# Kernel optimization log

Hardware: AMD Instinct MI355X
Metric: run time of the kernel (lower is better)

Reference implementation:

```python
import jax, jax.numpy as jnp
import numpy as np

B, N, C = 2, 32768, 512
L, H = 64, 8
DH = C // H
NB = N // L
EG_HID = 16


def setup_inputs() -> dict:
    key = jax.random.key(0)
    ks = jax.random.split(key, 12)
    x = jax.random.normal(ks[0], (B, N, C), dtype=jnp.float32)
    attn_mask = jax.random.randint(ks[1], (NB, L, L), 0, 2, dtype=jnp.int32)
    edge_feats = jax.random.normal(ks[2], (NB, L, L, 4), dtype=jnp.float32)
    s = 1.0 / np.sqrt(C)
    w_qkv = jax.random.normal(ks[3], (C, 3 * C), dtype=jnp.float32) * s
    b_qkv = jnp.zeros((3 * C,), dtype=jnp.float32)
    w_proj = jax.random.normal(ks[4], (C, C), dtype=jnp.float32) * s
    b_proj = jnp.zeros((C,), dtype=jnp.float32)
    w_eg1 = jax.random.normal(ks[5], (4, EG_HID), dtype=jnp.float32) * 0.01
    b_eg1 = jnp.zeros((EG_HID,), dtype=jnp.float32)
    w_eg2 = jax.random.normal(ks[6], (EG_HID, H), dtype=jnp.float32) * 0.01
    b_eg2 = jnp.zeros((H,), dtype=jnp.float32)
    w_blk = jax.random.normal(ks[7], (C, H), dtype=jnp.float32) * 0.01
    b_blk = jnp.zeros((H,), dtype=jnp.float32)
    return {"x": x, "attn_mask": attn_mask, "edge_feats": edge_feats,
            "w_qkv": w_qkv, "b_qkv": b_qkv, "w_proj": w_proj, "b_proj": b_proj,
            "w_eg1": w_eg1, "b_eg1": b_eg1, "w_eg2": w_eg2, "b_eg2": b_eg2,
            "w_blk": w_blk, "b_blk": b_blk}


def reference(x, attn_mask, edge_feats, w_qkv, b_qkv, w_proj, b_proj,
              w_eg1, b_eg1, w_eg2, b_eg2, w_blk, b_blk):
    scale = DH ** -0.5
    x_blk = x.reshape(B, NB, L, C)
    # bias_physics: (B, NB, L, L, 4), expanded across batch
    bias = jnp.broadcast_to(edge_feats[None], (B, NB, L, L, 4))
    idx = jnp.arange(L)
    # zero diagonal, set channel 3 of diagonal to 1
    bias = bias.at[:, :, idx, idx, :].set(0.0)
    bias = bias.at[:, :, idx, idx, 3].set(1.0)
    # mask: (B, NB, L, L); ensure each query row attends to at least itself
    mask = jnp.broadcast_to(attn_mask[None], (B, NB, L, L))
    need_diag = (mask.sum(axis=-1) < 1).astype(mask.dtype)  # (B, NB, L)
    diag = mask[:, :, idx, idx]
    mask = mask.at[:, :, idx, idx].set(jnp.maximum(diag, need_diag))
    # qkv
    qkv = x_blk @ w_qkv + b_qkv  # (B, NB, L, 3C)
    q = qkv[..., :C].reshape(B, NB, L, H, DH)
    k = qkv[..., C:2 * C].reshape(B, NB, L, H, DH)
    v = qkv[..., 2 * C:].reshape(B, NB, L, H, DH)
    scores = jnp.einsum('bnqhd,bnkhd->bnqkh', q, k) * scale
    scores = scores + bias[..., 3:4]
    mask_e = (mask[..., None] == 0)  # (B, NB, L, L, 1)
    scores = jnp.where(mask_e, -jnp.inf, scores)
    attn_probs = jax.nn.softmax(scores, axis=3)
    # edge-gate MLP: 4 -> 16 (exact GELU) -> H
    gate = jax.nn.gelu(bias @ w_eg1 + b_eg1, approximate=False) @ w_eg2 + b_eg2
    gate = jnp.where(mask_e, 0.0, gate)
    combined = attn_probs + gate
    x_mid = jnp.einsum('bnqkh,bnkhd->bnqhd', combined, v)  # (B, NB, L, H, DH)
    # block route token
    block_node = x_blk.mean(axis=2, keepdims=True)  # (B, NB, 1, C)
    v_block = (block_node @ w_qkv + b_qkv)[..., 2 * C:].reshape(B, NB, 1, H, DH)
    g_block = jax.nn.sigmoid(x_blk @ w_blk + b_blk)  # (B, NB, L, H)
    x_mid = x_mid + g_block[..., None] * v_block
    out = x_mid.reshape(B, NB, L, C) @ w_proj + b_proj
    return out.reshape(B, N, C)
```

## Files before the change

kernel.cpp:

```cpp
#include <hip/hip_runtime.h>

typedef unsigned short u16;
typedef __attribute__((ext_vector_type(8))) short bf16x8;
typedef __attribute__((ext_vector_type(4))) float f32x4;

#define NTOK 32768
#define CC 512
#define HH 8
#define LL 64
#define NBLK 512

__device__ __forceinline__ u16 f2bf(float f) {
    unsigned int u = __float_as_uint(f);
    unsigned int r = u + 0x7fffu + ((u >> 16) & 1u);
    return (u16)(r >> 16);
}
__device__ __forceinline__ float bf2f(u16 h) {
    return __uint_as_float(((unsigned int)h) << 16);
}
__device__ __forceinline__ bf16x8 bc8(uint4 v) {
    return __builtin_bit_cast(bf16x8, v);
}
__device__ __forceinline__ void dma16(const u16* g, u16* l) {
    __builtin_amdgcn_global_load_lds((const __attribute__((address_space(1))) void*)g,
                                     (__attribute__((address_space(3))) void*)l, 16, 0, 0);
}

__global__ __launch_bounds__(256) void convert_x_kernel(const float* __restrict__ x,
                                                        u16* __restrict__ xbf) {
    size_t i = ((size_t)blockIdx.x * 256 + threadIdx.x) * 8;
    const float4* p = (const float4*)(x + i);
    float4 a = p[0], b = p[1];
    uint4 o;
    o.x = (unsigned)f2bf(a.x) | ((unsigned)f2bf(a.y) << 16);
    o.y = (unsigned)f2bf(a.z) | ((unsigned)f2bf(a.w) << 16);
    o.z = (unsigned)f2bf(b.x) | ((unsigned)f2bf(b.y) << 16);
    o.w = (unsigned)f2bf(b.z) | ((unsigned)f2bf(b.w) << 16);
    *(uint4*)(xbf + i) = o;
}

__global__ __launch_bounds__(256) void transpose_bf16_kernel(const float* __restrict__ in,
                                                             u16* __restrict__ out,
                                                             int K, int Nn) {
    __shared__ float tile[32][33];
    int n0 = blockIdx.x * 32, k0 = blockIdx.y * 32;
    int tx = threadIdx.x & 31, ty = threadIdx.x >> 5;
#pragma unroll
    for (int i = 0; i < 4; ++i)
        tile[ty + i * 8][tx] = in[(size_t)(k0 + ty + i * 8) * Nn + n0 + tx];
    __syncthreads();
#pragma unroll
    for (int i = 0; i < 4; ++i)
        out[(size_t)(n0 + ty + i * 8) * K + k0 + tx] = f2bf(tile[tx][ty + i * 8]);
}

__global__ __launch_bounds__(256) void gate_sbias_kernel(const int* __restrict__ mask,
                                                         const float* __restrict__ edge,
                                                         const float* __restrict__ w1,
                                                         const float* __restrict__ b1,
                                                         const float* __restrict__ w2,
                                                         const float* __restrict__ b2,
                                                         u16* __restrict__ gate,
                                                         float* __restrict__ sbias) {
    __shared__ float w1s[64], b1s[16], w2s[128], b2s[8];
    __shared__ int nds[64];
    int t = threadIdx.x;
    int nb = blockIdx.x;
    if (t < 64) w1s[t] = w1[t];
    if (t < 16) b1s[t] = b1[t];
    if (t < 128) w2s[t] = w2[t];
    if (t < 8) b2s[t] = b2[t];
    if (t < 64) {
        int s = 0;
        const int* mr = mask + (size_t)(nb * 64 + t) * 64;
#pragma unroll 8
        for (int k = 0; k < 64; ++k) s += mr[k];
        nds[t] = (s < 1) ? 1 : 0;
    }
    __syncthreads();
#pragma unroll 1
    for (int it = 0; it < 16; ++it) {
        int p = it * 256 + t;
        int q = p >> 6, k = p & 63;
        int mv = mask[(size_t)(nb * 64 + q) * 64 + k];
        float e0, e1, e2, e3;
        if (q == k) {
            mv = max(mv, nds[q]);
            e0 = e1 = e2 = 0.f;
            e3 = 1.f;
        } else {
            const float* ep = edge + ((size_t)(nb * 64 + q) * 64 + k) * 4;
            e0 = ep[0]; e1 = ep[1]; e2 = ep[2]; e3 = ep[3];
        }
        sbias[(size_t)(nb * 64 + q) * 64 + k] = mv ? e3 : -1e30f;
        float g[8];
#pragma unroll
        for (int hh = 0; hh < 8; ++hh) g[hh] = b2s[hh];
#pragma unroll
        for (int j = 0; j < 16; ++j) {
            float hpre = e0 * w1s[j] + e1 * w1s[16 + j] + e2 * w1s[32 + j] + e3 * w1s[48 + j] + b1s[j];
            float hg = 0.5f * hpre * (1.f + erff(hpre * 0.70710678f));
#pragma unroll
            for (int hh = 0; hh < 8; ++hh) g[hh] += hg * w2s[j * 8 + hh];
        }
#pragma unroll
        for (int hh = 0; hh < 8; ++hh)
            gate[(((size_t)nb * 8 + hh) * 64 + q) * 64 + k] = f2bf(mv ? g[hh] : 0.f);
    }
}

__global__ __launch_bounds__(256) void gblock_kernel(const u16* __restrict__ xbf,
                                                     const float* __restrict__ w_blk,
                                                     const float* __restrict__ b_blk,
                                                     float* __restrict__ gbl) {
    __shared__ u16 Xs[32][520];
    __shared__ float wbs[512 * 8];
    __shared__ float bbs[8];
    int t = threadIdx.x;
    int tok0 = blockIdx.x * 32;
    for (int i = t; i < 4096; i += 256) wbs[i] = w_blk[i];
    if (t < 8) bbs[t] = b_blk[t];
    {
        int row = t >> 3, c0 = (t & 7) * 64;
        const uint4* src = (const uint4*)(xbf + (size_t)(tok0 + row) * 512 + c0);
        uint4* dst = (uint4*)(&Xs[row][c0]);
#pragma unroll
        for (int i = 0; i < 8; ++i) dst[i] = src[i];
    }
    __syncthreads();
    int row = t >> 3, h = t & 7;
    float acc = bbs[h];
#pragma unroll 8
    for (int c = 0; c < 512; ++c) acc += bf2f(Xs[row][c]) * wbs[c * 8 + h];
    gbl[(size_t)(tok0 + row) * 8 + h] = 1.f / (1.f + __expf(-acc));
}

__global__ __launch_bounds__(256) void qkv_gemm_kernel(const u16* __restrict__ xbf,
                                                       const u16* __restrict__ wqkvT,
                                                       const float* __restrict__ b_qkv,
                                                       u16* __restrict__ qkv) {
    __shared__ __align__(16) u16 As[128 * 64], Bs[128 * 64];
    int tid = threadIdx.x;
    int n0 = blockIdx.x * 128;
    int m0 = blockIdx.y * 128;
    int lane = tid & 63, l15 = lane & 15, quad = lane >> 4, wave = tid >> 6;
    int r8 = lane >> 3, jch = lane & 7;
    int js = jch ^ r8;
    int mwl = (wave >> 1) * 64, nwl = (wave & 1) * 64;
    int sw = l15 & 7;

    f32x4 acc[4][4];
#pragma unroll
    for (int i = 0; i < 4; ++i)
#pragma unroll
        for (int j = 0; j < 4; ++j) acc[i][j] = (f32x4){0.f, 0.f, 0.f, 0.f};

    int arow[4], brow[4];
#pragma unroll
    for (int i = 0; i < 4; ++i) arow[i] = (mwl + i * 16 + l15) * 64;
#pragma unroll
    for (int j = 0; j < 4; ++j) brow[j] = (nwl + j * 16 + l15) * 64;

    const u16* gA = xbf + (size_t)(m0 + wave * 32 + r8) * CC + js * 8;
    const u16* gB = wqkvT + (size_t)(n0 + wave * 32 + r8) * CC + js * 8;
    u16* lA = As + wave * 32 * 64;
    u16* lB = Bs + wave * 32 * 64;

    for (int kt = 0; kt < 8; ++kt) {
        int k0 = kt * 64;
#pragma unroll
        for (int t = 0; t < 4; ++t) {
            dma16(gA + (size_t)t * 8 * CC + k0, lA + t * 8 * 64);
            dma16(gB + (size_t)t * 8 * CC + k0, lB + t * 8 * 64);
        }
        __syncthreads();
#pragma unroll
        for (int kk = 0; kk < 2; ++kk) {
            int ch = ((kk * 4 + quad) ^ sw) * 8;
            bf16x8 a[4], bb[4];
#pragma unroll
            for (int i = 0; i < 4; ++i) a[i] = *(const bf16x8*)&As[arow[i] + ch];
#pragma unroll
            for (int j = 0; j < 4; ++j) bb[j] = *(const bf16x8*)&Bs[brow[j] + ch];
#pragma unroll
            for (int i = 0; i < 4; ++i)
#pragma unroll
                for (int j = 0; j < 4; ++j)
                    acc[i][j] = __builtin_amdgcn_mfma_f32_16x16x32_bf16(a[i], bb[j], acc[i][j], 0, 0, 0);
        }
        __syncthreads();
    }
#pragma unroll
    for (int i = 0; i < 4; ++i)
#pragma unroll
        for (int j = 0; j < 4; ++j) {
            int col = n0 + nwl + j * 16 + l15;
            float bp = b_qkv[col];
#pragma unroll
            for (int r = 0; r < 4; ++r) {
                int row = m0 + mwl + i * 16 + quad * 4 + r;
                qkv[(size_t)row * 1536 + col] = f2bf(acc[i][j][r] + bp);
            }
        }
}

__global__ __launch_bounds__(256) void outproj_kernel(const u16* __restrict__ xmid,
                                                      const u16* __restrict__ wprojT,
                                                      const float* __restrict__ b_proj,
                                                      float* __restrict__ out) {
    __shared__ __align__(16) u16 As[128 * 64], Bs[128 * 64];
    int tid = threadIdx.x;
    int n0 = blockIdx.x * 128;
    int m0 = blockIdx.y * 128;
    int lane = tid & 63, l15 = lane & 15, quad = lane >> 4, wave = tid >> 6;
    int r8 = lane >> 3, jch = lane & 7;
    int js = jch ^ r8;
    int mwl = (wave >> 1) * 64, nwl = (wave & 1) * 64;
    int sw = l15 & 7;

    f32x4 acc[4][4];
#pragma unroll
    for (int i = 0; i < 4; ++i)
#pragma unroll
        for (int j = 0; j < 4; ++j) acc[i][j] = (f32x4){0.f, 0.f, 0.f, 0.f};

    int arow[4], brow[4];
#pragma unroll
    for (int i = 0; i < 4; ++i) arow[i] = (mwl + i * 16 + l15) * 64;
#pragma unroll
    for (int j = 0; j < 4; ++j) brow[j] = (nwl + j * 16 + l15) * 64;

    const u16* gA = xmid + (size_t)(m0 + wave * 32 + r8) * CC + js * 8;
    const u16* gB = wprojT + (size_t)(n0 + wave * 32 + r8) * CC + js * 8;
    u16* lA = As + wave * 32 * 64;
    u16* lB = Bs + wave * 32 * 64;

    for (int kt = 0; kt < 8; ++kt) {
        int k0 = kt * 64;
#pragma unroll
        for (int t = 0; t < 4; ++t) {
            dma16(gA + (size_t)t * 8 * CC + k0, lA + t * 8 * 64);
            dma16(gB + (size_t)t * 8 * CC + k0, lB + t * 8 * 64);
        }
        __syncthreads();
#pragma unroll
        for (int kk = 0; kk < 2; ++kk) {
            int ch = ((kk * 4 + quad) ^ sw) * 8;
            bf16x8 a[4], bb[4];
#pragma unroll
            for (int i = 0; i < 4; ++i) a[i] = *(const bf16x8*)&As[arow[i] + ch];
#pragma unroll
            for (int j = 0; j < 4; ++j) bb[j] = *(const bf16x8*)&Bs[brow[j] + ch];
#pragma unroll
            for (int i = 0; i < 4; ++i)
#pragma unroll
                for (int j = 0; j < 4; ++j)
                    acc[i][j] = __builtin_amdgcn_mfma_f32_16x16x32_bf16(a[i], bb[j], acc[i][j], 0, 0, 0);
        }
        __syncthreads();
    }
#pragma unroll
    for (int i = 0; i < 4; ++i)
#pragma unroll
        for (int j = 0; j < 4; ++j) {
            int col = n0 + nwl + j * 16 + l15;
            float bp = b_proj[col];
#pragma unroll
            for (int r = 0; r < 4; ++r) {
                int row = m0 + mwl + i * 16 + quad * 4 + r;
                out[(size_t)row * CC + col] = acc[i][j][r] + bp;
            }
        }
}

__global__ __launch_bounds__(256) void attn_kernel(const u16* __restrict__ qkv,
                                                   const float* __restrict__ sbias,
                                                   const u16* __restrict__ gate,
                                                   const float* __restrict__ gbl,
                                                   u16* __restrict__ xmid) {
    __shared__ u16 VT[64 * 72], Ps[64 * 72];
    __shared__ float gl[64], vbl[64];
    int tid = threadIdx.x;
    int bid = blockIdx.x;
    int h = bid & 7, nb = (bid >> 3) & 511, b = bid >> 12;
    int lane = tid & 63, l15 = lane & 15, quad = lane >> 4, wave = tid >> 6;
    int m0 = wave * 16;
    size_t blockrow = (size_t)(b * NTOK + nb * 64);
    const u16* qbase = qkv + blockrow * 1536 + h * 64;

    {
        int key = tid & 63, d0 = (tid >> 6) * 16;
        const uint4* vsrc = (const uint4*)(qbase + (size_t)key * 1536 + 1024 + d0);
        uint4 v0 = vsrc[0], v1 = vsrc[1];
        u16 tmp[16];
        *(uint4*)tmp = v0;
        *(uint4*)(tmp + 8) = v1;
#pragma unroll
        for (int j = 0; j < 16; ++j) VT[(d0 + j) * 72 + key] = tmp[j];
    }
    if (tid < 64) gl[tid] = gbl[(blockrow + tid) * 8 + h];
    __syncthreads();

    if (tid < 64) {
        float s = 0.f;
#pragma unroll 8
        for (int k = 0; k < 64; ++k) s += bf2f(VT[tid * 72 + k]);
        vbl[tid] = s * 0.015625f;
    }

    f32x4 sc[4];
#pragma unroll
    for (int t = 0; t < 4; ++t) sc[t] = (f32x4){0.f, 0.f, 0.f, 0.f};
#pragma unroll
    for (int kk = 0; kk < 2; ++kk) {
        bf16x8 a = bc8(*(const uint4*)(qbase + (size_t)(m0 + l15) * 1536 + kk * 32 + quad * 8));
#pragma unroll
        for (int t = 0; t < 4; ++t) {
            bf16x8 bb = bc8(*(const uint4*)(qbase + (size_t)(t * 16 + l15) * 1536 + 512 + kk * 32 + quad * 8));
            sc[t] = __builtin_amdgcn_mfma_f32_16x16x32_bf16(a, bb, sc[t], 0, 0, 0);
        }
    }
    {
        const float* sbp = sbias + (size_t)nb * 64 * 64;
#pragma unroll
        for (int r = 0; r < 4; ++r) {
            int q = m0 + quad * 4 + r;
            float mx = -3e38f;
#pragma unroll
            for (int t = 0; t < 4; ++t) {
                float v = sc[t][r] * 0.125f + sbp[q * 64 + t * 16 + l15];
                sc[t][r] = v;
                mx = fmaxf(mx, v);
            }
            mx = fmaxf(mx, __shfl_xor(mx, 1));
            mx = fmaxf(mx, __shfl_xor(mx, 2));
            mx = fmaxf(mx, __shfl_xor(mx, 4));
            mx = fmaxf(mx, __shfl_xor(mx, 8));
            float sum = 0.f;
#pragma unroll
            for (int t = 0; t < 4; ++t) {
                float p = __expf(sc[t][r] - mx);
                sc[t][r] = p;
                sum += p;
            }
            sum += __shfl_xor(sum, 1);
            sum += __shfl_xor(sum, 2);
            sum += __shfl_xor(sum, 4);
            sum += __shfl_xor(sum, 8);
            float inv = 1.f / sum;
            const u16* gp = gate + (((size_t)nb * 8 + h) * 64 + q) * 64;
#pragma unroll
            for (int t = 0; t < 4; ++t) {
                float comb = sc[t][r] * inv + bf2f(gp[t * 16 + l15]);
                Ps[q * 72 + t * 16 + l15] = f2bf(comb);
            }
        }
    }
    __syncthreads();

    f32x4 o[4];
#pragma unroll
    for (int t = 0; t < 4; ++t) o[t] = (f32x4){0.f, 0.f, 0.f, 0.f};
#pragma unroll
    for (int kk = 0; kk < 2; ++kk) {
        bf16x8 a = *(const bf16x8*)&Ps[(m0 + l15) * 72 + kk * 32 + quad * 8];
#pragma unroll
        for (int t = 0; t < 4; ++t) {
            bf16x8 bb = *(const bf16x8*)&VT[(t * 16 + l15) * 72 + kk * 32 + quad * 8];
            o[t] = __builtin_amdgcn_mfma_f32_16x16x32_bf16(a, bb, o[t], 0, 0, 0);
        }
    }
#pragma unroll
    for (int t = 0; t < 4; ++t) {
#pragma unroll
        for (int r = 0; r < 4; ++r) {
            int q = m0 + quad * 4 + r, d = t * 16 + l15;
            float v = o[t][r] + gl[q] * vbl[d];
            xmid[(blockrow + q) * CC + h * 64 + d] = f2bf(v);
        }
    }
}

extern "C" void kernel_launch(void* const* d_in, const int* in_sizes, int n_in,
                              void* d_out, int out_size, void* d_ws, size_t ws_size,
                              hipStream_t stream) {
    const float* x = (const float*)d_in[0];
    const int* attn_mask = (const int*)d_in[1];
    const float* edge = (const float*)d_in[2];
    const float* w_qkv = (const float*)d_in[3];
    const float* b_qkv = (const float*)d_in[4];
    const float* w_proj = (const float*)d_in[5];
    const float* b_proj = (const float*)d_in[6];
    const float* w_eg1 = (const float*)d_in[7];
    const float* b_eg1 = (const float*)d_in[8];
    const float* w_eg2 = (const float*)d_in[9];
    const float* b_eg2 = (const float*)d_in[10];
    const float* w_blk = (const float*)d_in[11];
    const float* b_blk = (const float*)d_in[12];
    float* out = (float*)d_out;

    char* ws = (char*)d_ws;
    u16* xbf = (u16*)ws;
    u16* xmid = (u16*)ws;
    u16* qkv = (u16*)(ws + 67108864);
    u16* gate = (u16*)(ws + 268435456);
    float* sbias = (float*)(ws + 301989888);
    u16* wqkvT = (u16*)(ws + 310378496);
    u16* wprojT = (u16*)(ws + 311951360);
    float* gbl = (float*)(ws + 312475648);

    convert_x_kernel<<<16384, 256, 0, stream>>>(x, xbf);
    transpose_bf16_kernel<<<dim3(48, 16), 256, 0, stream>>>(w_qkv, wqkvT, 512, 1536);
    transpose_bf16_kernel<<<dim3(16, 16), 256, 0, stream>>>(w_proj, wprojT, 512, 512);
    gate_sbias_kernel<<<512, 256, 0, stream>>>(attn_mask, edge, w_eg1, b_eg1, w_eg2, b_eg2,
                                               gate, sbias);
    gblock_kernel<<<2048, 256, 0, stream>>>(xbf, w_blk, b_blk, gbl);
    qkv_gemm_kernel<<<dim3(12, 512), 256, 0, stream>>>(xbf, wqkvT, b_qkv, qkv);
    attn_kernel<<<8192, 256, 0, stream>>>(qkv, sbias, gate, gbl, xmid);
    outproj_kernel<<<dim3(4, 512), 256, 0, stream>>>(xmid, wprojT, b_proj, out);
}
```

Measured before the change: 717.2 us.

## Fuse block-gate GEMV into x conversion and pack bias/gate as permuted bf16

Removes the separate gblock kernel by computing the sigmoid block-gate inside the fp32-to-bf16 conversion kernel. Each wave handles one token, and the 8-head dot product is reduced with wave shuffles. The score bias becomes bf16 and, like the gate tensor, is stored in a permuted layout so each attention lane reads its four values with one ushort4 load instead of four scattered loads. The trade-off is that every conversion block now reloads the 16KB w_blk table into LDS, and the bias loses precision by going to bf16.

Result: no change. 715.2 us (-0.3%).

```diff
diff --git a/kernel.cpp b/kernel.cpp
--- a/kernel.cpp
+++ b/kernel.cpp
@@ -26,17 +26,45 @@
                                      (__attribute__((address_space(3))) void*)l, 16, 0, 0);
 }
 
-__global__ __launch_bounds__(256) void convert_x_kernel(const float* __restrict__ x,
-                                                        u16* __restrict__ xbf) {
-    size_t i = ((size_t)blockIdx.x * 256 + threadIdx.x) * 8;
-    const float4* p = (const float4*)(x + i);
+__global__ __launch_bounds__(256) void convert_gblock_kernel(const float* __restrict__ x,
+                                                             u16* __restrict__ xbf,
+                                                             const float* __restrict__ w_blk,
+                                                             const float* __restrict__ b_blk,
+                                                             float* __restrict__ gbl) {
+    __shared__ float wbs[4608];
+    int tid = threadIdx.x;
+    for (int i = tid; i < 4096; i += 256) wbs[i + (i >> 6)] = w_blk[i];
+    size_t tok = (size_t)blockIdx.x * 4 + (tid >> 6);
+    int lane = tid & 63;
+    int c0 = lane * 8;
+    const float4* p = (const float4*)(x + tok * CC + c0);
     float4 a = p[0], b = p[1];
     uint4 o;
     o.x = (unsigned)f2bf(a.x) | ((unsigned)f2bf(a.y) << 16);
     o.y = (unsigned)f2bf(a.z) | ((unsigned)f2bf(a.w) << 16);
     o.z = (unsigned)f2bf(b.x) | ((unsigned)f2bf(b.y) << 16);
     o.w = (unsigned)f2bf(b.z) | ((unsigned)f2bf(b.w) << 16);
-    *(uint4*)(xbf + i) = o;
+    *(uint4*)(xbf + tok * CC + c0) = o;
+    float xv[8] = {a.x, a.y, a.z, a.w, b.x, b.y, b.z, b.w};
+    __syncthreads();
+    float acc[8];
+#pragma unroll
+    for (int h = 0; h < 8; ++h) acc[h] = 0.f;
+#pragma unroll
+    for (int j = 0; j < 8; ++j) {
+        const float* wr = &wbs[(c0 + j) * 8 + lane];
+#pragma unroll
+        for (int h = 0; h < 8; ++h) acc[h] += xv[j] * wr[h];
+    }
+#pragma unroll
+    for (int h = 0; h < 8; ++h) {
+#pragma unroll
+        for (int off = 1; off < 64; off <<= 1) acc[h] += __shfl_xor(acc[h], off);
+    }
+    float v = acc[0];
+#pragma unroll
+    for (int h = 1; h < 8; ++h) v = (lane == h) ? acc[h] : v;
+    if (lane < 8) gbl[tok * 8 + lane] = 1.f / (1.f + __expf(-(v + b_blk[lane])));
 }
 
 __global__ __launch_bounds__(256) void transpose_bf16_kernel(const float* __restrict__ in,
@@ -60,8 +88,8 @@
                                                          const float* __restrict__ b1,
                                                          const float* __restrict__ w2,
                                                          const float* __restrict__ b2,
-                                                         u16* __restrict__ gate,
-                                                         float* __restrict__ sbias) {
+                                                         u16* __restrict__ gate2,
+                                                         u16* __restrict__ sbias2) {
     __shared__ float w1s[64], b1s[16], w2s[128], b2s[8];
     __shared__ int nds[64];
     int t = threadIdx.x;
@@ -82,6 +110,7 @@
     for (int it = 0; it < 16; ++it) {
         int p = it * 256 + t;
         int q = p >> 6, k = p & 63;
+        int pk = (k & 15) * 4 + (k >> 4);
         int mv = mask[(size_t)(nb * 64 + q) * 64 + k];
         float e0, e1, e2, e3;
         if (q == k) {
@@ -92,7 +121,7 @@
             const float* ep = edge + ((size_t)(nb * 64 + q) * 64 + k) * 4;
             e0 = ep[0]; e1 = ep[1]; e2 = ep[2]; e3 = ep[3];
         }
-        sbias[(size_t)(nb * 64 + q) * 64 + k] = mv ? e3 : -1e30f;
+        sbias2[(size_t)(nb * 64 + q) * 64 + pk] = f2bf(mv ? e3 : -1e30f);
         float g[8];
 #pragma unroll
         for (int hh = 0; hh < 8; ++hh) g[hh] = b2s[hh];
@@ -105,34 +134,8 @@
         }
 #pragma unroll
         for (int hh = 0; hh < 8; ++hh)
-            gate[(((size_t)nb * 8 + hh) * 64 + q) * 64 + k] = f2bf(mv ? g[hh] : 0.f);
-    }
-}
-
-__global__ __launch_bounds__(256) void gblock_kernel(const u16* __restrict__ xbf,
-                                                     const float* __restrict__ w_blk,
-                                                     const float* __restrict__ b_blk,
-                                                     float* __restrict__ gbl) {
-    __shared__ u16 Xs[32][520];
-    __shared__ float wbs[512 * 8];
-    __shared__ float bbs[8];
-    int t = threadIdx.x;
-    int tok0 = blockIdx.x * 32;
-    for (int i = t; i < 4096; i += 256) wbs[i] = w_blk[i];
-    if (t < 8) bbs[t] = b_blk[t];
-    {
-        int row = t >> 3, c0 = (t & 7) * 64;
-        const uint4* src = (const uint4*)(xbf + (size_t)(tok0 + row) * 512 + c0);
-        uint4* dst = (uint4*)(&Xs[row][c0]);
-#pragma unroll
-        for (int i = 0; i < 8; ++i) dst[i] = src[i];
-    }
-    __syncthreads();
-    int row = t >> 3, h = t & 7;
-    float acc = bbs[h];
-#pragma unroll 8
-    for (int c = 0; c < 512; ++c) acc += bf2f(Xs[row][c]) * wbs[c * 8 + h];
-    gbl[(size_t)(tok0 + row) * 8 + h] = 1.f / (1.f + __expf(-acc));
+            gate2[(((size_t)nb * 8 + hh) * 64 + q) * 64 + pk] = f2bf(mv ? g[hh] : 0.f);
+    }
 }
 
 __global__ __launch_bounds__(256) void qkv_gemm_kernel(const u16* __restrict__ xbf,
@@ -274,8 +277,8 @@
 }
 
 __global__ __launch_bounds__(256) void attn_kernel(const u16* __restrict__ qkv,
-                                                   const float* __restrict__ sbias,
-                                                   const u16* __restrict__ gate,
+                                                   const u16* __restrict__ sbias2,
+                                                   const u16* __restrict__ gate2,
                                                    const float* __restrict__ gbl,
                                                    u16* __restrict__ xmid) {
     __shared__ u16 VT[64 * 72], Ps[64 * 72];
@@ -321,14 +324,17 @@
         }
     }
     {
-        const float* sbp = sbias + (size_t)nb * 64 * 64;
+        const u16* sb2 = sbias2 + (size_t)nb * 4096;
+        const u16* gp2 = gate2 + ((size_t)nb * 8 + h) * 4096;
 #pragma unroll
         for (int r = 0; r < 4; ++r) {
             int q = m0 + quad * 4 + r;
+            ushort4 sv = *(const ushort4*)(sb2 + (q * 16 + l15) * 4);
+            float bias_t[4] = {bf2f(sv.x), bf2f(sv.y), bf2f(sv.z), bf2f(sv.w)};
             float mx = -3e38f;
 #pragma unroll
             for (int t = 0; t < 4; ++t) {
-                float v = sc[t][r] * 0.125f + sbp[q * 64 + t * 16 + l15];
+                float v = sc[t][r] * 0.125f + bias_t[t];
                 sc[t][r] = v;
                 mx = fmaxf(mx, v);
             }
@@ -348,10 +354,11 @@
             sum += __shfl_xor(sum, 4);
             sum += __shfl_xor(sum, 8);
             float inv = 1.f / sum;
-            const u16* gp = gate + (((size_t)nb * 8 + h) * 64 + q) * 64;
+            ushort4 gv = *(const ushort4*)(gp2 + (q * 16 + l15) * 4);
+            float gate_t[4] = {bf2f(gv.x), bf2f(gv.y), bf2f(gv.z), bf2f(gv.w)};
 #pragma unroll
             for (int t = 0; t < 4; ++t) {
-                float comb = sc[t][r] * inv + bf2f(gp[t * 16 + l15]);
+                float comb = sc[t][r] * inv + gate_t[t];
                 Ps[q * 72 + t * 16 + l15] = f2bf(comb);
             }
         }
@@ -403,19 +410,18 @@
     u16* xbf = (u16*)ws;
     u16* xmid = (u16*)ws;
     u16* qkv = (u16*)(ws + 67108864);
-    u16* gate = (u16*)(ws + 268435456);
-    float* sbias = (float*)(ws + 301989888);
-    u16* wqkvT = (u16*)(ws + 310378496);
-    u16* wprojT = (u16*)(ws + 311951360);
-    float* gbl = (float*)(ws + 312475648);
-
-    convert_x_kernel<<<16384, 256, 0, stream>>>(x, xbf);
+    u16* gate2 = (u16*)(ws + 268435456);
+    u16* sbias2 = (u16*)(ws + 301989888);
+    u16* wqkvT = (u16*)(ws + 306184192);
+    u16* wprojT = (u16*)(ws + 307757056);
+    float* gbl = (float*)(ws + 308281344);
+
+    convert_gblock_kernel<<<16384, 256, 0, stream>>>(x, xbf, w_blk, b_blk, gbl);
     transpose_bf16_kernel<<<dim3(48, 16), 256, 0, stream>>>(w_qkv, wqkvT, 512, 1536);
     transpose_bf16_kernel<<<dim3(16, 16), 256, 0, stream>>>(w_proj, wprojT, 512, 512);
     gate_sbias_kernel<<<512, 256, 0, stream>>>(attn_mask, edge, w_eg1, b_eg1, w_eg2, b_eg2,
-                                               gate, sbias);
-    gblock_kernel<<<2048, 256, 0, stream>>>(xbf, w_blk, b_blk, gbl);
+                                               gate2, sbias2);
     qkv_gemm_kernel<<<dim3(12, 512), 256, 0, stream>>>(xbf, wqkvT, b_qkv, qkv);
-    attn_kernel<<<8192, 256, 0, stream>>>(qkv, sbias, gate, gbl, xmid);
+    attn_kernel<<<8192, 256, 0, stream>>>(qkv, sbias2, gate2, gbl, xmid);
     outproj_kernel<<<dim3(4, 512), 256, 0, stream>>>(xmid, wprojT, b_proj, out);
 }
```
